# Kernel tuning notes

Measured on AMD Instinct MI355X. Metric: run time of the kernel, lower is better.

Reference implementation:

```python
import jax, jax.numpy as jnp
import numpy as np

B, N, U = 8, 2048, 256
BN_EPS = 1e-3  # keras BatchNormalization default epsilon
ADJ_DENSITY = 0.008  # ~16 neighbors per node on average


def setup_inputs() -> dict:
    key = jax.random.key(0)
    ks = jax.random.split(key, 16)
    s = 0.05  # weight scale ('random_normal' init is small-stddev in keras)
    x = jax.random.normal(ks[0], (B, N, U), jnp.float32)
    # sparse binary adjacency stored dense (per-sample SpMM pattern)
    adj = (jax.random.uniform(ks[1], (B, N, N)) < ADJ_DENSITY).astype(jnp.float32)
    nodal_mask = jnp.ones((B, N), jnp.float32)
    return {
        'x': x, 'adj': adj, 'nodal_mask': nodal_mask,
        'W_lin': jax.random.normal(ks[2], (U, U)) * s, 'b_lin': jnp.zeros((U,)),
        'Wq_mp': jax.random.normal(ks[3], (3, U, U)) * s, 'bq_mp': jnp.zeros((3, U)),
        'Wk_mp': jax.random.normal(ks[4], (3, U, U)) * s, 'bk_mp': jnp.zeros((3, U)),
        'Wv_mp': jax.random.normal(ks[5], (3, U, U)) * s, 'bv_mp': jnp.zeros((3, U)),
        'Wk_att': jax.random.normal(ks[6], (U, U)) * s,
        'Wv_att': jax.random.normal(ks[7], (U, U)) * s,
        'Wq_att': jax.random.normal(ks[8], (U, U)) * s,
        'Wo_att': jax.random.normal(ks[9], (U, U)) * s,
        'bn_gamma': jnp.ones((U,)), 'bn_beta': jnp.zeros((U,)),
        'bn_mean': jnp.zeros((U,)), 'bn_var': jnp.ones((U,)),
        'W_proj': jax.random.normal(ks[10], (U, U)) * s, 'b_proj': jnp.zeros((U,)),
        'W_res': jax.random.normal(ks[11], (U, U)) * s, 'b_res': jnp.zeros((U,)),
    }


def _dympn(x, adj, Ws, bs, mask):
    # 3 message-passing layers, each applied K_l=2 times (inference value)
    for i in range(3):
        for _ in range(2):
            xn = jnp.einsum('bmn,bnd->bmd', adj, x)  # batched SpMM (graph_conv mode)
            x = jax.nn.silu(jnp.einsum('bmd,de->bme', xn, Ws[i]) + bs[i])
    return x * mask[:, :, None]


def reference(x, adj, nodal_mask, W_lin, b_lin, Wq_mp, bq_mp, Wk_mp, bk_mp,
              Wv_mp, bv_mp, Wk_att, Wv_att, Wq_att, Wo_att,
              bn_gamma, bn_beta, bn_mean, bn_var, W_proj, b_proj, W_res, b_res):
    initial_x = x
    adj = jax.lax.stop_gradient(adj)
    h = jnp.einsum('bnd,de->bne', x, W_lin) + b_lin
    q = _dympn(h, adj, Wq_mp, bq_mp, nodal_mask)
    k = _dympn(h, adj, Wk_mp, bk_mp, nodal_mask)
    v = _dympn(h, adj, Wv_mp, bv_mp, nodal_mask)
    # linear attention
    m = nodal_mask[:, :, None]
    pk = jax.nn.silu(jnp.einsum('bnd,de->bne', k, Wk_att) * m)
    pv = jnp.einsum('bnd,de->bne', v, Wv_att) * m
    pq = jnp.einsum('bnd,de->bne', q, Wq_att)
    kv = jnp.einsum('bnd,bne->bde', pk, pv)       # [B,U,U]
    attn = jnp.einsum('bnd,bde->bne', pq, kv)
    attn = jnp.einsum('bnd,de->bne', attn, Wo_att)
    # batch norm (inference: moving stats) over last axis
    y = attn + initial_x
    y = bn_gamma * (y - bn_mean) * jax.lax.rsqrt(bn_var + BN_EPS) + bn_beta
    out = jax.nn.silu(jnp.einsum('bnd,de->bne', y, W_proj) + b_proj)
    out = out + jnp.einsum('bnd,de->bne', initial_x, W_res) + b_res
    out = out * nodal_mask[:, :, None]
    return out
```

## Files before the change

### kernel.cpp

```cpp
#include <hip/hip_runtime.h>
#include <stdint.h>

#define NB 8
#define NN 2048
#define NU 256
#define CAP 64
#define BNEPS 0.001f

typedef __attribute__((ext_vector_type(8))) short short8;
typedef __attribute__((ext_vector_type(4))) float floatx4;
typedef unsigned short u16;
typedef unsigned int u32;

__device__ __forceinline__ float bf2f(u16 u) {
  union { u32 i; float f; } c; c.i = ((u32)u) << 16; return c.f;
}
__device__ __forceinline__ u16 f2bf(float f) {
  union { float f; u32 i; } c; c.f = f;
  return (u16)((c.i + 0x7fffu + ((c.i >> 16) & 1u)) >> 16);
}
__device__ __forceinline__ void splitbf(float a, u16& h, u16& l) {
  h = f2bf(a);
  l = f2bf(a - bf2f(h));
}

enum : unsigned {
  F_BIAS = 2u, F_SILU = 4u, F_MASKPRE = 8u, F_MASKPOST = 16u,
  F_ADDX = 32u, F_BN = 64u, F_ADDT = 128u, F_ASHARED = 256u, F_BPERMAT = 512u,
  F_TPLANES = 1024u, F_OUTHL = 2048u
};

#define TP_MAT 524288
#define TP_LO  4194304
#define MSZ ((size_t)NN * NU)

__global__ __launch_bounds__(256) void build_nbr_k(
    const float* __restrict__ adj, int* __restrict__ cnt, int* __restrict__ idx)
{
  int row = blockIdx.x;
  const float* base = adj + (size_t)row * NN;
  __shared__ int c;
  if (threadIdx.x == 0) c = 0;
  __syncthreads();
#pragma unroll
  for (int j = 0; j < 8; j++) {
    int n = j * 256 + threadIdx.x;
    if (base[n] != 0.f) {
      int p = atomicAdd(&c, 1);
      if (p < CAP) idx[(size_t)row * CAP + p] = n;
    }
  }
  __syncthreads();
  if (threadIdx.x == 0) cnt[row] = (c < CAP ? c : CAP);
}

struct WPtrs { const float* p[16]; };

__global__ __launch_bounds__(256) void conv_w_k(WPtrs wp, u16* __restrict__ dst)
{
  int gid = blockIdx.x * 256 + threadIdx.x;
  int mat = gid >> 13;
  int rem = gid & 8191;
  int kb = rem >> 10;
  int n = (rem >> 2) & 255;
  int slot = rem & 3;
  int qv = (slot - (n >> 1)) & 3;
  int k0 = kb * 32 + qv * 8;
  const float* W = wp.p[mat];
  u32 oh[4], ol[4];
#pragma unroll
  for (int t2 = 0; t2 < 4; t2++) {
    float f0 = W[(size_t)(k0 + 2 * t2) * 256 + n];
    float f1 = W[(size_t)(k0 + 2 * t2 + 1) * 256 + n];
    u16 h0, l0, h1, l1;
    splitbf(f0, h0, l0);
    splitbf(f1, h1, l1);
    oh[t2] = (u32)h0 | ((u32)h1 << 16);
    ol[t2] = (u32)l0 | ((u32)l1 << 16);
  }
  uint4 qh; qh.x = oh[0]; qh.y = oh[1]; qh.z = oh[2]; qh.w = oh[3];
  uint4 ql; ql.x = ol[0]; ql.y = ol[1]; ql.z = ol[2]; ql.w = ol[3];
  *(uint4*)(dst + (size_t)gid * 8) = qh;
  *(uint4*)(dst + 1048576 + (size_t)gid * 8) = ql;
}

__global__ __launch_bounds__(256) void conv_x_k(
    const float* __restrict__ x, u16* __restrict__ dst, size_t oLo)
{
  size_t i = ((size_t)blockIdx.x * 256 + threadIdx.x) * 4;
  float4 v = *(const float4*)(x + i);
  u16 h0, l0, h1, l1, h2, l2, h3, l3;
  splitbf(v.x, h0, l0); splitbf(v.y, h1, l1);
  splitbf(v.z, h2, l2); splitbf(v.w, h3, l3);
  uint2 H; H.x = (u32)h0 | ((u32)h1 << 16); H.y = (u32)h2 | ((u32)h3 << 16);
  uint2 L; L.x = (u32)l0 | ((u32)l1 << 16); L.y = (u32)l2 | ((u32)l3 << 16);
  *(uint2*)(dst + i) = H;
  *(uint2*)(dst + oLo + i) = L;
}

template <unsigned F, int NG>
__global__ __launch_bounds__(512, 4) void gemm_k(
    const u16* __restrict__ Abase, size_t aLo,
    const u16* __restrict__ W0, const u16* __restrict__ W1, const u16* __restrict__ W2,
    size_t wLo,
    const float* __restrict__ b0, const float* __restrict__ b1, const float* __restrict__ b2,
    const float* __restrict__ mask,
    const float* __restrict__ xf32,
    const float* __restrict__ gma, const float* __restrict__ bta,
    const float* __restrict__ bmu, const float* __restrict__ bvr,
    const float* __restrict__ addt,
    void* __restrict__ outp, size_t oLo)
{
  const int tid = threadIdx.x;
  const int id = blockIdx.x;
  const int xcd = id & 7;
  const int t = id >> 3;
  const int chain = (NG == 1) ? 0 : (t % NG);
  const int xt = (NG == 1) ? t : (t / NG);
  const int mat = chain * 8 + xcd;
  const int b = xcd;
  const int bm = xt * 64;

  __shared__ alignas(16) u16 Ah[64 * 264];
  __shared__ alignas(16) u16 Al[64 * 264];

  const u16* Whi = (F & F_BPERMAT) ? (W0 + (size_t)mat * 65536)
                                   : (chain == 0 ? W0 : (chain == 1 ? W1 : W2));
  const u16* Wlo = Whi + wLo;
  const float* bsel = (chain == 0 ? b0 : (chain == 1 ? b1 : b2));
  const u16* Ahp = Abase + ((F & F_ASHARED) ? (size_t)b : (size_t)mat) * MSZ;
  const u16* Alp = Ahp + aLo;

#pragma unroll
  for (int s = tid; s < 1024; s += 512) {
    int r = s >> 4;
    int c = (s & 15) << 4;
    size_t ao = (size_t)(bm + r) * 256 + c;
    *(uint4*)&Ah[r * 264 + c] = *(const uint4*)(Ahp + ao);
    *(uint4*)&Ah[r * 264 + c + 8] = *(const uint4*)(Ahp + ao + 8);
    *(uint4*)&Al[r * 264 + c] = *(const uint4*)(Alp + ao);
    *(uint4*)&Al[r * 264 + c + 8] = *(const uint4*)(Alp + ao + 8);
  }
  __syncthreads();

  const int lane = tid & 63;
  const int w = tid >> 6;
  const int wr = w >> 2;
  const int wc = w & 3;
  const int m16 = lane & 15;
  const int q = lane >> 4;

  floatx4 acc[2][4];
#pragma unroll
  for (int i = 0; i < 2; i++)
#pragma unroll
    for (int j = 0; j < 4; j++) acc[i][j] = (floatx4){0.f, 0.f, 0.f, 0.f};

#pragma unroll
  for (int kk = 0; kk < 8; kk++) {
    short8 bh[4], bl2[4];
#pragma unroll
    for (int nt = 0; nt < 4; nt++) {
      int n = wc * 64 + nt * 16 + m16;
      size_t off = (size_t)kk * 8192 + (size_t)n * 32 + (size_t)(((q + (n >> 1)) & 3) * 8);
      bh[nt] = *(const short8*)(Whi + off);
      bl2[nt] = *(const short8*)(Wlo + off);
    }
#pragma unroll
    for (int mt = 0; mt < 2; mt++) {
      int row = wr * 32 + mt * 16 + m16;
      short8 ah = *(const short8*)&Ah[row * 264 + kk * 32 + q * 8];
      short8 al2 = *(const short8*)&Al[row * 264 + kk * 32 + q * 8];
#pragma unroll
      for (int nt = 0; nt < 4; nt++) {
        acc[mt][nt] = __builtin_amdgcn_mfma_f32_16x16x32_bf16(ah, bh[nt], acc[mt][nt], 0, 0, 0);
        acc[mt][nt] = __builtin_amdgcn_mfma_f32_16x16x32_bf16(al2, bh[nt], acc[mt][nt], 0, 0, 0);
        acc[mt][nt] = __builtin_amdgcn_mfma_f32_16x16x32_bf16(ah, bl2[nt], acc[mt][nt], 0, 0, 0);
      }
    }
  }

#pragma unroll
  for (int mt = 0; mt < 2; mt++) {
    if (F & F_TPLANES) {
      u16* oh = (u16*)outp + (size_t)b * TP_MAT;
      u16* ol = oh + TP_LO;
      int gr0 = bm + wr * 32 + mt * 16 + q * 4;
#pragma unroll
      for (int nt = 0; nt < 4; nt++) {
        int col = wc * 64 + nt * 16 + m16;
        u16 hh[4], ll[4];
#pragma unroll
        for (int r = 0; r < 4; r++) {
          float t2 = acc[mt][nt][r];
          float mv = mask[b * NN + gr0 + r];
          if (F & F_MASKPRE) t2 *= mv;
          if (F & F_SILU) t2 = t2 / (1.f + __expf(-t2));
          if (F & F_MASKPOST) t2 *= mv;
          splitbf(t2, hh[r], ll[r]);
        }
        uint2 H2, L2v;
        H2.x = (u32)hh[0] | ((u32)hh[1] << 16);
        H2.y = (u32)hh[2] | ((u32)hh[3] << 16);
        L2v.x = (u32)ll[0] | ((u32)ll[1] << 16);
        L2v.y = (u32)ll[2] | ((u32)ll[3] << 16);
        *(uint2*)(oh + (size_t)col * 2048 + gr0) = H2;
        *(uint2*)(ol + (size_t)col * 2048 + gr0) = L2v;
      }
    } else {
#pragma unroll
      for (int r = 0; r < 4; r++) {
        int gr = bm + wr * 32 + mt * 16 + q * 4 + r;
        float mval = 1.f;
        if (F & (F_MASKPRE | F_MASKPOST)) mval = mask[b * NN + gr];
#pragma unroll
        for (int nt = 0; nt < 4; nt++) {
          int col = wc * 64 + nt * 16 + m16;
          float t2 = acc[mt][nt][r];
          if (F & F_BIAS) t2 += bsel[col];
          if (F & F_MASKPRE) t2 *= mval;
          if (F & F_SILU) t2 = t2 / (1.f + __expf(-t2));
          if (F & F_ADDX) t2 += xf32[((size_t)b * NN + gr) * NU + col];
          if (F & F_BN) t2 = gma[col] * (t2 - bmu[col]) * rsqrtf(bvr[col] + BNEPS) + bta[col];
          if (F & F_ADDT) t2 += addt[((size_t)mat * NN + gr) * NU + col];
          if (F & F_MASKPOST) t2 *= mval;
          size_t o = ((size_t)mat * NN + gr) * NU + col;
          if (F & F_OUTHL) {
            u16 h0, l0;
            splitbf(t2, h0, l0);
            ((u16*)outp)[o] = h0;
            ((u16*)outp)[o + oLo] = l0;
          } else {
            ((float*)outp)[o] = t2;
          }
        }
      }
    }
  }
}

template <unsigned F>
__global__ __launch_bounds__(256, 8) void agg_k(
    const float* __restrict__ g, u16* __restrict__ xo, size_t oLo,
    const float* __restrict__ bq, const float* __restrict__ bk, const float* __restrict__ bv,
    const float* __restrict__ mask,
    const int* __restrict__ ncnt, const int* __restrict__ nidx)
{
  int id = blockIdx.x;
  int c3 = id >> 12;
  int sub = id & 4095;
  int b = sub & 7;
  int rg = sub >> 3;
  int tid = threadIdx.x;
  int w = tid >> 6;
  int l = tid & 63;
  int row = rg * 4 + w;
  int rowid = b * NN + row;
  const float* __restrict__ gm = g + ((size_t)c3 * 8 + b) * MSZ;
  const float* bias = (c3 == 0) ? bq : (c3 == 1 ? bk : bv);
  int cnt = ncnt[rowid];
  const int* __restrict__ ip = nidx + (size_t)rowid * CAP;
  int c = l * 4;
  float4 a; a.x = a.y = a.z = a.w = 0.f;
  int e = 0;
  for (; e + 4 <= cnt; e += 4) {
    int4 i4 = *(const int4*)(ip + e);
    float4 v0 = *(const float4*)(gm + ((size_t)i4.x << 8) + c);
    float4 v1 = *(const float4*)(gm + ((size_t)i4.y << 8) + c);
    float4 v2 = *(const float4*)(gm + ((size_t)i4.z << 8) + c);
    float4 v3 = *(const float4*)(gm + ((size_t)i4.w << 8) + c);
    a.x += v0.x + v1.x + v2.x + v3.x;
    a.y += v0.y + v1.y + v2.y + v3.y;
    a.z += v0.z + v1.z + v2.z + v3.z;
    a.w += v0.w + v1.w + v2.w + v3.w;
  }
  for (; e < cnt; e++) {
    float4 v = *(const float4*)(gm + ((size_t)ip[e] << 8) + c);
    a.x += v.x; a.y += v.y; a.z += v.z; a.w += v.w;
  }
  float4 bb = *(const float4*)(bias + c);
  float o[4] = {a.x + bb.x, a.y + bb.y, a.z + bb.z, a.w + bb.w};
  float mv = (F & F_MASKPOST) ? mask[rowid] : 1.f;
  u16 hh[4], ll[4];
#pragma unroll
  for (int j = 0; j < 4; j++) {
    float t = o[j];
    if (F & F_SILU) t = t / (1.f + __expf(-t));
    if (F & F_MASKPOST) t *= mv;
    splitbf(t, hh[j], ll[j]);
  }
  uint2 H; H.x = (u32)hh[0] | ((u32)hh[1] << 16); H.y = (u32)hh[2] | ((u32)hh[3] << 16);
  uint2 L; L.x = (u32)ll[0] | ((u32)ll[1] << 16); L.y = (u32)ll[2] | ((u32)ll[3] << 16);
  size_t o0 = ((size_t)c3 * 8 + b) * MSZ + ((size_t)row << 8) + c;
  *(uint2*)(xo + o0) = H;
  *(uint2*)(xo + oLo + o0) = L;
}

__global__ __launch_bounds__(256, 2) void kv_k(
    const u16* __restrict__ pkT, const u16* __restrict__ pvT, float* __restrict__ part)
{
  int et = blockIdx.x * 128;
  int dt = blockIdx.y * 128;
  int z = blockIdx.z;
  int b = z & 7;
  int p = z >> 3;
  int tid = threadIdx.x;
  int lane = tid & 63, w = tid >> 6;
  int m16 = lane & 15, q = lane >> 4;

  const u16* pkh = pkT + (size_t)b * TP_MAT;
  const u16* pkl = pkh + TP_LO;
  const u16* pvh = pvT + (size_t)b * TP_MAT;
  const u16* pvl = pvh + TP_LO;

  int d_base = dt + (w >> 1) * 64 + m16;
  int e_base = et + (w & 1) * 64 + m16;

  floatx4 acc[4][4];
#pragma unroll
  for (int i = 0; i < 4; i++)
#pragma unroll
    for (int j = 0; j < 4; j++) acc[i][j] = (floatx4){0.f, 0.f, 0.f, 0.f};

#pragma unroll
  for (int kt = 0; kt < 8; kt++) {
    int kc = p * 256 + kt * 32 + q * 8;
    short8 ah[4], al[4], bh[4], bl[4];
#pragma unroll
    for (int mt = 0; mt < 4; mt++) {
      size_t o = (size_t)(d_base + mt * 16) * 2048 + kc;
      ah[mt] = *(const short8*)(pkh + o);
      al[mt] = *(const short8*)(pkl + o);
    }
#pragma unroll
    for (int nt = 0; nt < 4; nt++) {
      size_t o = (size_t)(e_base + nt * 16) * 2048 + kc;
      bh[nt] = *(const short8*)(pvh + o);
      bl[nt] = *(const short8*)(pvl + o);
    }
#pragma unroll
    for (int mt = 0; mt < 4; mt++)
#pragma unroll
      for (int nt = 0; nt < 4; nt++) {
        acc[mt][nt] = __builtin_amdgcn_mfma_f32_16x16x32_bf16(ah[mt], bh[nt], acc[mt][nt], 0, 0, 0);
        acc[mt][nt] = __builtin_amdgcn_mfma_f32_16x16x32_bf16(al[mt], bh[nt], acc[mt][nt], 0, 0, 0);
        acc[mt][nt] = __builtin_amdgcn_mfma_f32_16x16x32_bf16(ah[mt], bl[nt], acc[mt][nt], 0, 0, 0);
      }
  }

#pragma unroll
  for (int mt = 0; mt < 4; mt++)
#pragma unroll
    for (int r = 0; r < 4; r++) {
      int d = dt + (w >> 1) * 64 + mt * 16 + q * 4 + r;
#pragma unroll
      for (int nt = 0; nt < 4; nt++) {
        int e = et + (w & 1) * 64 + nt * 16 + m16;
        part[(size_t)z * 65536 + (size_t)d * 256 + e] = acc[mt][nt][r];
      }
    }
}

__global__ __launch_bounds__(256) void kv_conv_k(const float* __restrict__ part, u16* __restrict__ dst)
{
  int gid = blockIdx.x * 256 + threadIdx.x;
  int b = gid >> 13;
  int rem = gid & 8191;
  int kb = rem >> 10;
  int e = (rem >> 2) & 255;
  int slot = rem & 3;
  int qv = (slot - (e >> 1)) & 3;
  int d0 = kb * 32 + qv * 8;
  const float* src = part + (size_t)b * 65536 + (size_t)d0 * 256 + e;
  u32 oh[4], ol[4];
#pragma unroll
  for (int t2 = 0; t2 < 4; t2++) {
    float s0 = 0.f, s1 = 0.f;
#pragma unroll
    for (int pp = 0; pp < 8; pp++) {
      const float* sp = src + (size_t)pp * 524288 + t2 * 512;
      s0 += sp[0];
      s1 += sp[256];
    }
    u16 h0, l0, h1, l1;
    splitbf(s0, h0, l0);
    splitbf(s1, h1, l1);
    oh[t2] = (u32)h0 | ((u32)h1 << 16);
    ol[t2] = (u32)l0 | ((u32)l1 << 16);
  }
  uint4 qh; qh.x = oh[0]; qh.y = oh[1]; qh.z = oh[2]; qh.w = oh[3];
  uint4 ql; ql.x = ol[0]; ql.y = ol[1]; ql.z = ol[2]; ql.w = ol[3];
  *(uint4*)(dst + (size_t)gid * 8) = qh;
  *(uint4*)(dst + 524288 + (size_t)gid * 8) = ql;
}

extern "C" void kernel_launch(void* const* d_in, const int* in_sizes, int n_in,
                              void* d_out, int out_size, void* d_ws, size_t ws_size,
                              hipStream_t stream)
{
  const float* x = (const float*)d_in[0];
  const float* adj = (const float*)d_in[1];
  const float* mask = (const float*)d_in[2];
  const float* W_lin = (const float*)d_in[3];
  const float* b_lin = (const float*)d_in[4];
  const float* Wq_mp = (const float*)d_in[5];
  const float* bq_mp = (const float*)d_in[6];
  const float* Wk_mp = (const float*)d_in[7];
  const float* bk_mp = (const float*)d_in[8];
  const float* Wv_mp = (const float*)d_in[9];
  const float* bv_mp = (const float*)d_in[10];
  const float* Wk_att = (const float*)d_in[11];
  const float* Wv_att = (const float*)d_in[12];
  const float* Wq_att = (const float*)d_in[13];
  const float* Wo_att = (const float*)d_in[14];
  const float* bn_gamma = (const float*)d_in[15];
  const float* bn_beta = (const float*)d_in[16];
  const float* bn_mean = (const float*)d_in[17];
  const float* bn_var = (const float*)d_in[18];
  const float* W_proj = (const float*)d_in[19];
  const float* b_proj = (const float*)d_in[20];
  const float* W_res = (const float*)d_in[21];
  const float* b_res = (const float*)d_in[22];

  char* ws = (char*)d_ws;
  int* CNT    = (int*)(ws + 0);
  int* IDX    = (int*)(ws + (1ull << 20));
  u16* WSZ    = (u16*)(ws + (5ull << 20));
  u16* KVS    = (u16*)(ws + (9ull << 20));
  float* KVP  = (float*)(ws + (11ull << 20));
  u16* XHL    = (u16*)(ws + (27ull << 20));
  u16* HHL    = (u16*)(ws + (43ull << 20));
  float* G    = (float*)(ws + (59ull << 20));
  u16* XA     = (u16*)(ws + (107ull << 20));
  u16* XB     = (u16*)(ws + (155ull << 20));

  const size_t WLO = 1048576;
  const size_t KLO = 524288;
  const size_t A8  = 8 * MSZ;
  const size_t A24 = 24 * MSZ;

  u16* PQHL = HHL;
  u16* PKT = (u16*)G;
  u16* PVT = (u16*)((char*)G + (16ull << 20));
  u16* ATT = (u16*)((char*)G + (32ull << 20));
  u16* YHL = XA;
  float* TMP = (float*)((char*)XA + (16ull << 20));

  WPtrs wp;
  wp.p[0] = W_lin;
  wp.p[1] = Wq_mp; wp.p[2] = Wq_mp + 65536; wp.p[3] = Wq_mp + 131072;
  wp.p[4] = Wk_mp; wp.p[5] = Wk_mp + 65536; wp.p[6] = Wk_mp + 131072;
  wp.p[7] = Wv_mp; wp.p[8] = Wv_mp + 65536; wp.p[9] = Wv_mp + 131072;
  wp.p[10] = Wk_att; wp.p[11] = Wv_att; wp.p[12] = Wq_att; wp.p[13] = Wo_att;
  wp.p[14] = W_proj; wp.p[15] = W_res;
  conv_w_k<<<512, 256, 0, stream>>>(wp, WSZ);
  conv_x_k<<<4096, 256, 0, stream>>>(x, XHL, A8);
  build_nbr_k<<<NB * NN, 256, 0, stream>>>(adj, CNT, IDX);

  gemm_k<F_BIAS | F_OUTHL, 1><<<256, 512, 0, stream>>>(XHL, A8,
      WSZ, nullptr, nullptr, WLO, b_lin, nullptr, nullptr, nullptr, nullptr,
      bn_gamma, bn_beta, bn_mean, bn_var, nullptr, HHL, A8);

  u16* xbufs[2] = {XA, XB};
  for (int s = 0; s < 6; s++) {
    int i = s >> 1;
    const u16* Wq_s = WSZ + (size_t)(1 + i) * 65536;
    const u16* Wk_s = WSZ + (size_t)(4 + i) * 65536;
    const u16* Wv_s = WSZ + (size_t)(7 + i) * 65536;
    u16* inb = (s == 0) ? HHL : xbufs[(s + 1) & 1];
    u16* ob = xbufs[s & 1];
    if (s == 0)
      gemm_k<F_ASHARED, 3><<<768, 512, 0, stream>>>(HHL, A8,
          Wq_s, Wk_s, Wv_s, WLO, nullptr, nullptr, nullptr, nullptr, nullptr,
          bn_gamma, bn_beta, bn_mean, bn_var, nullptr, G, 0);
    else
      gemm_k<0u, 3><<<768, 512, 0, stream>>>(inb, A24,
          Wq_s, Wk_s, Wv_s, WLO, nullptr, nullptr, nullptr, nullptr, nullptr,
          bn_gamma, bn_beta, bn_mean, bn_var, nullptr, G, 0);
    const float* bq = bq_mp + i * 256;
    const float* bk = bk_mp + i * 256;
    const float* bv = bv_mp + i * 256;
    if (s == 5)
      agg_k<F_BIAS | F_SILU | F_MASKPOST><<<12288, 256, 0, stream>>>(
          G, ob, A24, bq, bk, bv, mask, CNT, IDX);
    else
      agg_k<F_BIAS | F_SILU><<<12288, 256, 0, stream>>>(
          G, ob, A24, bq, bk, bv, mask, CNT, IDX);
  }

  gemm_k<F_OUTHL, 1><<<256, 512, 0, stream>>>(XB, A24,
      WSZ + (size_t)12 * 65536, nullptr, nullptr, WLO,
      nullptr, nullptr, nullptr, nullptr, nullptr,
      bn_gamma, bn_beta, bn_mean, bn_var, nullptr, PQHL, A8);
  gemm_k<F_SILU | F_MASKPRE | F_TPLANES, 1><<<256, 512, 0, stream>>>(XB + 8 * MSZ, A24,
      WSZ + (size_t)10 * 65536, nullptr, nullptr, WLO,
      nullptr, nullptr, nullptr, mask, nullptr,
      bn_gamma, bn_beta, bn_mean, bn_var, nullptr, PKT, 0);
  gemm_k<F_MASKPOST | F_TPLANES, 1><<<256, 512, 0, stream>>>(XB + 16 * MSZ, A24,
      WSZ + (size_t)11 * 65536, nullptr, nullptr, WLO,
      nullptr, nullptr, nullptr, mask, nullptr,
      bn_gamma, bn_beta, bn_mean, bn_var, nullptr, PVT, 0);

  kv_k<<<dim3(2, 2, 64), 256, 0, stream>>>(PKT, PVT, KVP);
  kv_conv_k<<<256, 256, 0, stream>>>(KVP, KVS);

  gemm_k<F_BPERMAT | F_OUTHL, 1><<<256, 512, 0, stream>>>(PQHL, A8,
      KVS, nullptr, nullptr, KLO,
      nullptr, nullptr, nullptr, nullptr, nullptr,
      bn_gamma, bn_beta, bn_mean, bn_var, nullptr, ATT, A8);

  gemm_k<F_ADDX | F_BN | F_OUTHL, 1><<<256, 512, 0, stream>>>(ATT, A8,
      WSZ + (size_t)13 * 65536, nullptr, nullptr, WLO,
      nullptr, nullptr, nullptr, nullptr, x,
      bn_gamma, bn_beta, bn_mean, bn_var, nullptr, YHL, A8);

  gemm_k<F_BIAS, 1><<<256, 512, 0, stream>>>(XHL, A8,
      WSZ + (size_t)15 * 65536, nullptr, nullptr, WLO,
      b_res, nullptr, nullptr, nullptr, nullptr,
      bn_gamma, bn_beta, bn_mean, bn_var, nullptr, TMP, 0);

  gemm_k<F_BIAS | F_SILU | F_ADDT | F_MASKPOST, 1><<<256, 512, 0, stream>>>(YHL, A8,
      WSZ + (size_t)14 * 65536, nullptr, nullptr, WLO,
      b_proj, nullptr, nullptr, mask, nullptr,
      bn_gamma, bn_beta, bn_mean, bn_var, TMP, d_out, 0);

  (void)in_sizes; (void)n_in; (void)out_size; (void)ws_size;
}
```

Measured before the change: 846.3 us.

## Fuse pq/pk/pv projections into one launch and remap GEMM warp tiling

The GEMM kernel now takes per-chain A, weight and output pointers, with a separate epilogue flag set for each chain. This lets the three attention projections (q, k, v) run as one 768-block launch instead of three 256-block launches. The per-warp tile also changes from 2x4 to 4x2 (each of the 8 warps covers all 64 rows and a 32-column slice), so each wave now loads fewer B fragments and more A fragments from LDS. The aim is to cut launch count and fill the GPU better; the risks are epilogue branch divergence by chain and different LDS/global traffic from the new warp layout.

After: 823.0 us. 2.8% less time.

```diff
diff --git a/kernel.cpp b/kernel.cpp
--- a/kernel.cpp
+++ b/kernel.cpp
@@ -26,7 +26,7 @@
 
 enum : unsigned {
   F_BIAS = 2u, F_SILU = 4u, F_MASKPRE = 8u, F_MASKPOST = 16u,
-  F_ADDX = 32u, F_BN = 64u, F_ADDT = 128u, F_ASHARED = 256u, F_BPERMAT = 512u,
+  F_ADDX = 32u, F_BN = 64u, F_ADDT = 128u, F_BPERMAT = 512u,
   F_TPLANES = 1024u, F_OUTHL = 2048u
 };
 
@@ -98,97 +98,24 @@
   *(uint2*)(dst + oLo + i) = L;
 }
 
-template <unsigned F, int NG>
-__global__ __launch_bounds__(512, 4) void gemm_k(
-    const u16* __restrict__ Abase, size_t aLo,
-    const u16* __restrict__ W0, const u16* __restrict__ W1, const u16* __restrict__ W2,
-    size_t wLo,
-    const float* __restrict__ b0, const float* __restrict__ b1, const float* __restrict__ b2,
-    const float* __restrict__ mask,
+template <unsigned F>
+__device__ __forceinline__ void gemm_epi(
+    floatx4 (&acc)[4][2], int b, int bm, int w, int m16, int q,
+    const float* __restrict__ bias, const float* __restrict__ mask,
     const float* __restrict__ xf32,
     const float* __restrict__ gma, const float* __restrict__ bta,
     const float* __restrict__ bmu, const float* __restrict__ bvr,
-    const float* __restrict__ addt,
-    void* __restrict__ outp, size_t oLo)
-{
-  const int tid = threadIdx.x;
-  const int id = blockIdx.x;
-  const int xcd = id & 7;
-  const int t = id >> 3;
-  const int chain = (NG == 1) ? 0 : (t % NG);
-  const int xt = (NG == 1) ? t : (t / NG);
-  const int mat = chain * 8 + xcd;
-  const int b = xcd;
-  const int bm = xt * 64;
-
-  __shared__ alignas(16) u16 Ah[64 * 264];
-  __shared__ alignas(16) u16 Al[64 * 264];
-
-  const u16* Whi = (F & F_BPERMAT) ? (W0 + (size_t)mat * 65536)
-                                   : (chain == 0 ? W0 : (chain == 1 ? W1 : W2));
-  const u16* Wlo = Whi + wLo;
-  const float* bsel = (chain == 0 ? b0 : (chain == 1 ? b1 : b2));
-  const u16* Ahp = Abase + ((F & F_ASHARED) ? (size_t)b : (size_t)mat) * MSZ;
-  const u16* Alp = Ahp + aLo;
-
-#pragma unroll
-  for (int s = tid; s < 1024; s += 512) {
-    int r = s >> 4;
-    int c = (s & 15) << 4;
-    size_t ao = (size_t)(bm + r) * 256 + c;
-    *(uint4*)&Ah[r * 264 + c] = *(const uint4*)(Ahp + ao);
-    *(uint4*)&Ah[r * 264 + c + 8] = *(const uint4*)(Ahp + ao + 8);
-    *(uint4*)&Al[r * 264 + c] = *(const uint4*)(Alp + ao);
-    *(uint4*)&Al[r * 264 + c + 8] = *(const uint4*)(Alp + ao + 8);
-  }
-  __syncthreads();
-
-  const int lane = tid & 63;
-  const int w = tid >> 6;
-  const int wr = w >> 2;
-  const int wc = w & 3;
-  const int m16 = lane & 15;
-  const int q = lane >> 4;
-
-  floatx4 acc[2][4];
-#pragma unroll
-  for (int i = 0; i < 2; i++)
-#pragma unroll
-    for (int j = 0; j < 4; j++) acc[i][j] = (floatx4){0.f, 0.f, 0.f, 0.f};
-
-#pragma unroll
-  for (int kk = 0; kk < 8; kk++) {
-    short8 bh[4], bl2[4];
-#pragma unroll
-    for (int nt = 0; nt < 4; nt++) {
-      int n = wc * 64 + nt * 16 + m16;
-      size_t off = (size_t)kk * 8192 + (size_t)n * 32 + (size_t)(((q + (n >> 1)) & 3) * 8);
-      bh[nt] = *(const short8*)(Whi + off);
-      bl2[nt] = *(const short8*)(Wlo + off);
-    }
-#pragma unroll
-    for (int mt = 0; mt < 2; mt++) {
-      int row = wr * 32 + mt * 16 + m16;
-      short8 ah = *(const short8*)&Ah[row * 264 + kk * 32 + q * 8];
-      short8 al2 = *(const short8*)&Al[row * 264 + kk * 32 + q * 8];
-#pragma unroll
-      for (int nt = 0; nt < 4; nt++) {
-        acc[mt][nt] = __builtin_amdgcn_mfma_f32_16x16x32_bf16(ah, bh[nt], acc[mt][nt], 0, 0, 0);
-        acc[mt][nt] = __builtin_amdgcn_mfma_f32_16x16x32_bf16(al2, bh[nt], acc[mt][nt], 0, 0, 0);
-        acc[mt][nt] = __builtin_amdgcn_mfma_f32_16x16x32_bf16(ah, bl2[nt], acc[mt][nt], 0, 0, 0);
-      }
-    }
-  }
-
-#pragma unroll
-  for (int mt = 0; mt < 2; mt++) {
+    const float* __restrict__ addt, void* __restrict__ outp, size_t oLo)
+{
+#pragma unroll
+  for (int mt = 0; mt < 4; mt++) {
     if (F & F_TPLANES) {
       u16* oh = (u16*)outp + (size_t)b * TP_MAT;
       u16* ol = oh + TP_LO;
-      int gr0 = bm + wr * 32 + mt * 16 + q * 4;
-#pragma unroll
-      for (int nt = 0; nt < 4; nt++) {
-        int col = wc * 64 + nt * 16 + m16;
+      int gr0 = bm + mt * 16 + q * 4;
+#pragma unroll
+      for (int nt = 0; nt < 2; nt++) {
+        int col = w * 32 + nt * 16 + m16;
         u16 hh[4], ll[4];
 #pragma unroll
         for (int r = 0; r < 4; r++) {
@@ -210,21 +137,21 @@
     } else {
 #pragma unroll
       for (int r = 0; r < 4; r++) {
-        int gr = bm + wr * 32 + mt * 16 + q * 4 + r;
+        int gr = bm + mt * 16 + q * 4 + r;
         float mval = 1.f;
         if (F & (F_MASKPRE | F_MASKPOST)) mval = mask[b * NN + gr];
 #pragma unroll
-        for (int nt = 0; nt < 4; nt++) {
-          int col = wc * 64 + nt * 16 + m16;
+        for (int nt = 0; nt < 2; nt++) {
+          int col = w * 32 + nt * 16 + m16;
           float t2 = acc[mt][nt][r];
-          if (F & F_BIAS) t2 += bsel[col];
+          if (F & F_BIAS) t2 += bias[col];
           if (F & F_MASKPRE) t2 *= mval;
           if (F & F_SILU) t2 = t2 / (1.f + __expf(-t2));
           if (F & F_ADDX) t2 += xf32[((size_t)b * NN + gr) * NU + col];
           if (F & F_BN) t2 = gma[col] * (t2 - bmu[col]) * rsqrtf(bvr[col] + BNEPS) + bta[col];
-          if (F & F_ADDT) t2 += addt[((size_t)mat * NN + gr) * NU + col];
+          if (F & F_ADDT) t2 += addt[((size_t)b * NN + gr) * NU + col];
           if (F & F_MASKPOST) t2 *= mval;
-          size_t o = ((size_t)mat * NN + gr) * NU + col;
+          size_t o = ((size_t)b * NN + gr) * NU + col;
           if (F & F_OUTHL) {
             u16 h0, l0;
             splitbf(t2, h0, l0);
@@ -237,6 +164,96 @@
       }
     }
   }
+}
+
+template <int NG, unsigned F0, unsigned F1, unsigned F2>
+__global__ __launch_bounds__(512, 4) void gemm_k(
+    const u16* __restrict__ A0, const u16* __restrict__ A1, const u16* __restrict__ A2,
+    size_t aLo,
+    const u16* __restrict__ W0, const u16* __restrict__ W1, const u16* __restrict__ W2,
+    size_t wLo,
+    const float* __restrict__ b0, const float* __restrict__ b1, const float* __restrict__ b2,
+    const float* __restrict__ mask,
+    const float* __restrict__ xf32,
+    const float* __restrict__ gma, const float* __restrict__ bta,
+    const float* __restrict__ bmu, const float* __restrict__ bvr,
+    const float* __restrict__ addt,
+    void* __restrict__ o0, void* __restrict__ o1, void* __restrict__ o2,
+    size_t oLo)
+{
+  const int tid = threadIdx.x;
+  const int id = blockIdx.x;
+  const int xcd = id & 7;
+  const int t = id >> 3;
+  const int chain = (NG == 1) ? 0 : (t % NG);
+  const int xt = (NG == 1) ? t : (t / NG);
+  const int b = xcd;
+  const int bm = xt * 64;
+
+  __shared__ alignas(16) u16 Ah[64 * 264];
+  __shared__ alignas(16) u16 Al[64 * 264];
+
+  const u16* Abase = (chain == 0) ? A0 : (chain == 1 ? A1 : A2);
+  const u16* Wsel = (chain == 0) ? W0 : (chain == 1 ? W1 : W2);
+  if (F0 & F_BPERMAT) Wsel = W0 + (size_t)b * 65536;
+  const u16* Whi = Wsel;
+  const u16* Wlo = Whi + wLo;
+  const u16* Ahp = Abase + (size_t)b * MSZ;
+  const u16* Alp = Ahp + aLo;
+
+#pragma unroll
+  for (int s = tid; s < 1024; s += 512) {
+    int r = s >> 4;
+    int c = (s & 15) << 4;
+    size_t ao = (size_t)(bm + r) * 256 + c;
+    *(uint4*)&Ah[r * 264 + c] = *(const uint4*)(Ahp + ao);
+    *(uint4*)&Ah[r * 264 + c + 8] = *(const uint4*)(Ahp + ao + 8);
+    *(uint4*)&Al[r * 264 + c] = *(const uint4*)(Alp + ao);
+    *(uint4*)&Al[r * 264 + c + 8] = *(const uint4*)(Alp + ao + 8);
+  }
+  __syncthreads();
+
+  const int lane = tid & 63;
+  const int w = tid >> 6;
+  const int m16 = lane & 15;
+  const int q = lane >> 4;
+
+  floatx4 acc[4][2];
+#pragma unroll
+  for (int i = 0; i < 4; i++)
+#pragma unroll
+    for (int j = 0; j < 2; j++) acc[i][j] = (floatx4){0.f, 0.f, 0.f, 0.f};
+
+#pragma unroll
+  for (int kk = 0; kk < 8; kk++) {
+    short8 bh[2], bl2[2];
+#pragma unroll
+    for (int nt = 0; nt < 2; nt++) {
+      int n = w * 32 + nt * 16 + m16;
+      size_t off = (size_t)kk * 8192 + (size_t)n * 32 + (size_t)(((q + (n >> 1)) & 3) * 8);
+      bh[nt] = *(const short8*)(Whi + off);
+      bl2[nt] = *(const short8*)(Wlo + off);
+    }
+#pragma unroll
+    for (int mt = 0; mt < 4; mt++) {
+      int row = mt * 16 + m16;
+      short8 ah = *(const short8*)&Ah[row * 264 + kk * 32 + q * 8];
+      short8 al2 = *(const short8*)&Al[row * 264 + kk * 32 + q * 8];
+#pragma unroll
+      for (int nt = 0; nt < 2; nt++) {
+        acc[mt][nt] = __builtin_amdgcn_mfma_f32_16x16x32_bf16(ah, bh[nt], acc[mt][nt], 0, 0, 0);
+        acc[mt][nt] = __builtin_amdgcn_mfma_f32_16x16x32_bf16(al2, bh[nt], acc[mt][nt], 0, 0, 0);
+        acc[mt][nt] = __builtin_amdgcn_mfma_f32_16x16x32_bf16(ah, bl2[nt], acc[mt][nt], 0, 0, 0);
+      }
+    }
+  }
+
+  if (NG == 1 || chain == 0)
+    gemm_epi<F0>(acc, b, bm, w, m16, q, b0, mask, xf32, gma, bta, bmu, bvr, addt, o0, oLo);
+  else if (chain == 1)
+    gemm_epi<F1>(acc, b, bm, w, m16, q, b1, mask, xf32, gma, bta, bmu, bvr, addt, o1, oLo);
+  else
+    gemm_epi<F2>(acc, b, bm, w, m16, q, b2, mask, xf32, gma, bta, bmu, bvr, addt, o2, oLo);
 }
 
 template <unsigned F>
@@ -457,9 +474,11 @@
   conv_x_k<<<4096, 256, 0, stream>>>(x, XHL, A8);
   build_nbr_k<<<NB * NN, 256, 0, stream>>>(adj, CNT, IDX);
 
-  gemm_k<F_BIAS | F_OUTHL, 1><<<256, 512, 0, stream>>>(XHL, A8,
-      WSZ, nullptr, nullptr, WLO, b_lin, nullptr, nullptr, nullptr, nullptr,
-      bn_gamma, bn_beta, bn_mean, bn_var, nullptr, HHL, A8);
+  gemm_k<1, F_BIAS | F_OUTHL, 0u, 0u><<<256, 512, 0, stream>>>(
+      XHL, XHL, XHL, A8, WSZ, WSZ, WSZ, WLO,
+      b_lin, nullptr, nullptr, mask, nullptr,
+      bn_gamma, bn_beta, bn_mean, bn_var, nullptr,
+      HHL, nullptr, nullptr, A8);
 
   u16* xbufs[2] = {XA, XB};
   for (int s = 0; s < 6; s++) {
@@ -468,15 +487,16 @@
     const u16* Wk_s = WSZ + (size_t)(4 + i) * 65536;
     const u16* Wv_s = WSZ + (size_t)(7 + i) * 65536;
     u16* inb = (s == 0) ? HHL : xbufs[(s + 1) & 1];
+    size_t aLo = (s == 0) ? A8 : A24;
+    const u16* Aq = inb;
+    const u16* Ak = (s == 0) ? inb : inb + 8 * MSZ;
+    const u16* Av = (s == 0) ? inb : inb + 16 * MSZ;
     u16* ob = xbufs[s & 1];
-    if (s == 0)
-      gemm_k<F_ASHARED, 3><<<768, 512, 0, stream>>>(HHL, A8,
-          Wq_s, Wk_s, Wv_s, WLO, nullptr, nullptr, nullptr, nullptr, nullptr,
-          bn_gamma, bn_beta, bn_mean, bn_var, nullptr, G, 0);
-    else
-      gemm_k<0u, 3><<<768, 512, 0, stream>>>(inb, A24,
-          Wq_s, Wk_s, Wv_s, WLO, nullptr, nullptr, nullptr, nullptr, nullptr,
-          bn_gamma, bn_beta, bn_mean, bn_var, nullptr, G, 0);
+    gemm_k<3, 0u, 0u, 0u><<<768, 512, 0, stream>>>(
+        Aq, Ak, Av, aLo, Wq_s, Wk_s, Wv_s, WLO,
+        nullptr, nullptr, nullptr, mask, nullptr,
+        bn_gamma, bn_beta, bn_mean, bn_var, nullptr,
+        G, G + 8 * MSZ, G + 16 * MSZ, 0);
     const float* bq = bq_mp + i * 256;
     const float* bk = bk_mp + i * 256;
     const float* bv = bv_mp + i * 256;
@@ -488,41 +508,43 @@
           G, ob, A24, bq, bk, bv, mask, CNT, IDX);
   }
 
-  gemm_k<F_OUTHL, 1><<<256, 512, 0, stream>>>(XB, A24,
-      WSZ + (size_t)12 * 65536, nullptr, nullptr, WLO,
-      nullptr, nullptr, nullptr, nullptr, nullptr,
-      bn_gamma, bn_beta, bn_mean, bn_var, nullptr, PQHL, A8);
-  gemm_k<F_SILU | F_MASKPRE | F_TPLANES, 1><<<256, 512, 0, stream>>>(XB + 8 * MSZ, A24,
-      WSZ + (size_t)10 * 65536, nullptr, nullptr, WLO,
+  gemm_k<3, F_OUTHL, F_SILU | F_MASKPRE | F_TPLANES, F_MASKPOST | F_TPLANES>
+      <<<768, 512, 0, stream>>>(
+      XB, XB + 8 * MSZ, XB + 16 * MSZ, A24,
+      WSZ + (size_t)12 * 65536, WSZ + (size_t)10 * 65536, WSZ + (size_t)11 * 65536, WLO,
       nullptr, nullptr, nullptr, mask, nullptr,
-      bn_gamma, bn_beta, bn_mean, bn_var, nullptr, PKT, 0);
-  gemm_k<F_MASKPOST | F_TPLANES, 1><<<256, 512, 0, stream>>>(XB + 16 * MSZ, A24,
-      WSZ + (size_t)11 * 65536, nullptr, nullptr, WLO,
-      nullptr, nullptr, nullptr, mask, nullptr,
-      bn_gamma, bn_beta, bn_mean, bn_var, nullptr, PVT, 0);
+      bn_gamma, bn_beta, bn_mean, bn_var, nullptr,
+      PQHL, PKT, PVT, A8);
 
   kv_k<<<dim3(2, 2, 64), 256, 0, stream>>>(PKT, PVT, KVP);
   kv_conv_k<<<256, 256, 0, stream>>>(KVP, KVS);
 
-  gemm_k<F_BPERMAT | F_OUTHL, 1><<<256, 512, 0, stream>>>(PQHL, A8,
-      KVS, nullptr, nullptr, KLO,
-      nullptr, nullptr, nullptr, nullptr, nullptr,
-      bn_gamma, bn_beta, bn_mean, bn_var, nullptr, ATT, A8);
-
-  gemm_k<F_ADDX | F_BN | F_OUTHL, 1><<<256, 512, 0, stream>>>(ATT, A8,
+  gemm_k<1, F_BPERMAT | F_OUTHL, 0u, 0u><<<256, 512, 0, stream>>>(
+      PQHL, PQHL, PQHL, A8, KVS, KVS, KVS, KLO,
+      nullptr, nullptr, nullptr, mask, nullptr,
+      bn_gamma, bn_beta, bn_mean, bn_var, nullptr,
+      ATT, nullptr, nullptr, A8);
+
+  gemm_k<1, F_ADDX | F_BN | F_OUTHL, 0u, 0u><<<256, 512, 0, stream>>>(
+      ATT, ATT, ATT, A8,
       WSZ + (size_t)13 * 65536, nullptr, nullptr, WLO,
-      nullptr, nullptr, nullptr, nullptr, x,
-      bn_gamma, bn_beta, bn_mean, bn_var, nullptr, YHL, A8);
-
-  gemm_k<F_BIAS, 1><<<256, 512, 0, stream>>>(XHL, A8,
+      nullptr, nullptr, nullptr, mask, x,
+      bn_gamma, bn_beta, bn_mean, bn_var, nullptr,
+      YHL, nullptr, nullptr, A8);
+
+  gemm_k<1, F_BIAS, 0u, 0u><<<256, 512, 0, stream>>>(
+      XHL, XHL, XHL, A8,
       WSZ + (size_t)15 * 65536, nullptr, nullptr, WLO,
-      b_res, nullptr, nullptr, nullptr, nullptr,
-      bn_gamma, bn_beta, bn_mean, bn_var, nullptr, TMP, 0);
-
-  gemm_k<F_BIAS | F_SILU | F_ADDT | F_MASKPOST, 1><<<256, 512, 0, stream>>>(YHL, A8,
+      b_res, nullptr, nullptr, mask, nullptr,
+      bn_gamma, bn_beta, bn_mean, bn_var, nullptr,
+      TMP, nullptr, nullptr, 0);
+
+  gemm_k<1, F_BIAS | F_SILU | F_ADDT | F_MASKPOST, 0u, 0u><<<256, 512, 0, stream>>>(
+      YHL, YHL, YHL, A8,
       WSZ + (size_t)14 * 65536, nullptr, nullptr, WLO,
       b_proj, nullptr, nullptr, mask, nullptr,
-      bn_gamma, bn_beta, bn_mean, bn_var, TMP, d_out, 0);
+      bn_gamma, bn_beta, bn_mean, bn_var, TMP,
+      d_out, nullptr, nullptr, 0);
 
   (void)in_sizes; (void)n_in; (void)out_size; (void)ws_size;
 }
```
